# Optimization experiments

Hardware: AMD Instinct MI355X
Metric: run time of the kernel (lower is better)

The kernel has to match this reference:

```python
import jax, jax.numpy as jnp
import numpy as np

B, T, D, H = 16, 2048, 512, 512  # batch, seq_len, input_dim, hidden_dim


def setup_inputs() -> dict:
    key = jax.random.key(0)
    k1, k2, k3 = jax.random.split(key, 3)
    x = jax.random.normal(k1, (B, T, D), dtype=jnp.float32)
    # vanilla tanh RnnCell parameters
    W_xh = jax.random.normal(k2, (D, H), dtype=jnp.float32) / np.float32(np.sqrt(D))
    W_hh = jax.random.normal(k3, (H, H), dtype=jnp.float32) / np.float32(np.sqrt(H))
    b = jnp.zeros((H,), dtype=jnp.float32)
    # DFA feedback matrix, 'diagonal' init branch: diag(linspace(0,1,H))
    A = jnp.diag(jnp.linspace(0.0, 1.0, H).astype(jnp.float32))
    return {"x": x, "W_xh": W_xh, "W_hh": W_hh, "b": b, "A": A}


def reference(x, W_xh, W_hh, b, A):
    # Forward of DfaRnn: sequential RNN loop. detach() does not change forward
    # values, so this is a plain tanh RNN scan. A only affects the backward.
    Bb = x.shape[0]
    h0 = jnp.zeros((Bb, W_hh.shape[0]), dtype=x.dtype)

    def step(h, xt):
        h_new = jnp.tanh(xt @ W_xh + h @ W_hh + b)
        return h_new, h_new

    _, hs = jax.lax.scan(step, h0, jnp.swapaxes(x, 0, 1))  # [T,B,H]
    return jnp.swapaxes(hs, 0, 1)  # [B,T,H]
```

## Files before the change

### kernel.cpp

```cpp
#include <hip/hip_runtime.h>
#include <cmath>

#define B_ 16
#define T_ 2048
#define D_ 512
#define H_ 512

__global__ __launch_bounds__(256) void gemm_xw(
    const float* __restrict__ x,
    const float* __restrict__ Wxh,
    const float* __restrict__ bias,
    float* __restrict__ out)
{
    const int tid = threadIdx.x;
    const int n0 = blockIdx.x * 128;
    const int m0 = blockIdx.y * 128;

    __shared__ float As[8][132];
    __shared__ float Bs[8][132];

    const int tx = tid & 15, ty = tid >> 4;
    float acc[8][8] = {};

    const int arow = tid >> 1;
    const int akq  = (tid & 1) * 4;
    const int brow = tid >> 5;
    const int bcol = (tid & 31) * 4;

    for (int k0 = 0; k0 < D_; k0 += 8) {
        float4 a4 = *(const float4*)(x + (size_t)(m0 + arow) * D_ + k0 + akq);
        float4 b4 = *(const float4*)(Wxh + (size_t)(k0 + brow) * H_ + n0 + bcol);
        __syncthreads();
        As[akq + 0][arow] = a4.x;
        As[akq + 1][arow] = a4.y;
        As[akq + 2][arow] = a4.z;
        As[akq + 3][arow] = a4.w;
        *(float4*)(&Bs[brow][bcol]) = b4;
        __syncthreads();
#pragma unroll
        for (int kk = 0; kk < 8; ++kk) {
            float4 a0 = *(const float4*)(&As[kk][ty * 8]);
            float4 a1 = *(const float4*)(&As[kk][ty * 8 + 4]);
            float4 b0 = *(const float4*)(&Bs[kk][tx * 8]);
            float4 b1 = *(const float4*)(&Bs[kk][tx * 8 + 4]);
            float a_[8] = {a0.x, a0.y, a0.z, a0.w, a1.x, a1.y, a1.z, a1.w};
            float b_[8] = {b0.x, b0.y, b0.z, b0.w, b1.x, b1.y, b1.z, b1.w};
#pragma unroll
            for (int i = 0; i < 8; ++i)
#pragma unroll
                for (int j = 0; j < 8; ++j) acc[i][j] += a_[i] * b_[j];
        }
    }

    const float4 bv0 = *(const float4*)(bias + n0 + tx * 8);
    const float4 bv1 = *(const float4*)(bias + n0 + tx * 8 + 4);
    const float bb[8] = {bv0.x, bv0.y, bv0.z, bv0.w, bv1.x, bv1.y, bv1.z, bv1.w};
#pragma unroll
    for (int i = 0; i < 8; ++i) {
        const int m = m0 + ty * 8 + i;
        float4 o0, o1;
        o0.x = acc[i][0] + bb[0]; o0.y = acc[i][1] + bb[1];
        o0.z = acc[i][2] + bb[2]; o0.w = acc[i][3] + bb[3];
        o1.x = acc[i][4] + bb[4]; o1.y = acc[i][5] + bb[5];
        o1.z = acc[i][6] + bb[6]; o1.w = acc[i][7] + bb[7];
        *(float4*)(out + (size_t)m * H_ + n0 + tx * 8)     = o0;
        *(float4*)(out + (size_t)m * H_ + n0 + tx * 8 + 4) = o1;
    }
}

__device__ __forceinline__ void bar_lds() {
    asm volatile("s_waitcnt lgkmcnt(0)\n\ts_barrier" ::: "memory");
}

__global__ __launch_bounds__(512, 2) void rnn_rec(
    const float* __restrict__ Whh,
    float* __restrict__ out,
    unsigned long long* __restrict__ ws)
{
    const int tid = threadIdx.x;
    const int b = blockIdx.x & 15;
    const int s = blockIdx.x >> 4;
    const int j = tid & 63;
    const int p = tid >> 6;
    const int col = (s << 6) + j;

    __shared__ float h_lds[H_];
    __shared__ float part[8 * 64];

    float W_reg[64];
    {
        const float* wbase = Whh + (size_t)(p * 64) * H_ + col;
#pragma unroll
        for (int r = 0; r < 64; ++r) {
            const float* addr = wbase + (size_t)r * H_;
            asm volatile("global_load_dword %0, %1, off"
                         : "=v"(W_reg[r]) : "v"(addr));
        }
        asm volatile("s_waitcnt vmcnt(0)" ::: "memory");
    }

    h_lds[tid] = 0.0f;
    __syncthreads();

    float* outb = out + (size_t)b * T_ * H_;
    unsigned long long* wsb = ws + (size_t)b * 2 * H_;

    float xw0 = 0.0f, xw1 = 0.0f, xw2 = 0.0f;
    if (p == 0) {
        xw0 = outb[(size_t)0 * H_ + col];
        xw1 = outb[(size_t)1 * H_ + col];
        xw2 = outb[(size_t)2 * H_ + col];
    }

    for (int t = 0; t < T_; ++t) {
        float acc = 0.0f;
        const float4* hv = (const float4*)(h_lds + (p << 6));
#pragma unroll
        for (int i = 0; i < 16; ++i) {
            float4 h4 = hv[i];
            acc += h4.x * W_reg[4 * i + 0];
            acc += h4.y * W_reg[4 * i + 1];
            acc += h4.z * W_reg[4 * i + 2];
            acc += h4.w * W_reg[4 * i + 3];
        }
        part[tid] = acc;
        bar_lds();

        const unsigned int tag = (unsigned int)(t + 1);
        const int slot = (t + 1) & 1;
        unsigned long long* wslot = wsb + (size_t)slot * H_;

        if (p == 0) {
            asm volatile("s_waitcnt vmcnt(0)" ::: "memory");
            float ssum = xw0;
#pragma unroll
            for (int q = 0; q < 8; ++q) ssum += part[q * 64 + j];
            union { unsigned int u; float f; } cv;
            cv.f = tanhf(ssum);
            unsigned long long pv =
                ((unsigned long long)tag << 32) | (unsigned long long)cv.u;
            __hip_atomic_store(wslot + col, pv, __ATOMIC_RELAXED,
                               __HIP_MEMORY_SCOPE_AGENT);
            outb[(size_t)t * H_ + col] = cv.f;
            h_lds[col] = cv.f;
            xw0 = xw1;
            xw1 = xw2;
            xw2 = (t + 3 < T_) ? outb[(size_t)(t + 3) * H_ + col] : 0.0f;
        } else {
            const int q = (p == s) ? 0 : p;
            unsigned long long* src = wslot + (q << 6) + j;
            unsigned long long v;
            do {
                v = __hip_atomic_load(src, __ATOMIC_RELAXED,
                                      __HIP_MEMORY_SCOPE_AGENT);
            } while ((unsigned int)(v >> 32) < tag);
            union { unsigned int u; float f; } cv;
            cv.u = (unsigned int)v;
            h_lds[(q << 6) + j] = cv.f;
        }
        bar_lds();
    }
}

extern "C" void kernel_launch(void* const* d_in, const int* in_sizes, int n_in,
                              void* d_out, int out_size, void* d_ws,
                              size_t ws_size, hipStream_t stream) {
    const float* x    = (const float*)d_in[0];
    const float* Wxh  = (const float*)d_in[1];
    const float* Whh  = (const float*)d_in[2];
    const float* bias = (const float*)d_in[3];
    float* out = (float*)d_out;

    hipMemsetAsync(d_ws, 0, (size_t)B_ * 2 * H_ * sizeof(unsigned long long),
                   stream);

    dim3 ggrid(H_ / 128, (B_ * T_) / 128, 1);
    gemm_xw<<<ggrid, 256, 0, stream>>>(x, Wxh, bias, out);

    rnn_rec<<<128, 512, 0, stream>>>(Whh, out, (unsigned long long*)d_ws);
}
```

Baseline: 2.966 ms.

## Restructure RNN step to one barrier with a distributed shuffle reduction

The per-step recurrence is reorganised. Every wave now polls the global exchange buffer for its own 64-element slice of h at the start of the step, so each wave only reads h values it wrote itself and the second block barrier goes away. The cross-wave partial-sum reduction is spread over all waves using a transposed LDS read plus xor shuffles, rather than being done serially by wave 0. The partial buffer and the xw prefetch are double-buffered in LDS to stay safe with a single barrier. In exchange, every wave now polls global memory, and correctness depends on subtle LDS ordering across steps.

```diff
diff --git a/kernel.cpp b/kernel.cpp
--- a/kernel.cpp
+++ b/kernel.cpp
@@ -75,21 +75,21 @@
 __global__ __launch_bounds__(512, 2) void rnn_rec(
     const float* __restrict__ Whh,
     float* __restrict__ out,
-    unsigned long long* __restrict__ ws)
+    unsigned long long* __restrict__ ex)
 {
     const int tid = threadIdx.x;
     const int b = blockIdx.x & 15;
     const int s = blockIdx.x >> 4;
-    const int j = tid & 63;
+    const int l = tid & 63;
     const int p = tid >> 6;
-    const int col = (s << 6) + j;
 
     __shared__ float h_lds[H_];
-    __shared__ float part[8 * 64];
+    __shared__ float part[2][8 * 68];
+    __shared__ float xw_lds[2][64];
 
     float W_reg[64];
     {
-        const float* wbase = Whh + (size_t)(p * 64) * H_ + col;
+        const float* wbase = Whh + (size_t)(p * 64) * H_ + (s * 64 + l);
 #pragma unroll
         for (int r = 0; r < 64; ++r) {
             const float* addr = wbase + (size_t)r * H_;
@@ -99,20 +99,36 @@
         asm volatile("s_waitcnt vmcnt(0)" ::: "memory");
     }
 
+    float* outb = out + (size_t)b * T_ * H_;
+    unsigned long long* exb = ex + (size_t)b * 2 * H_;
+
     h_lds[tid] = 0.0f;
+    if (tid < 128) {
+        const int tt = tid >> 6;
+        const int c  = tid & 63;
+        xw_lds[tt][c] = outb[(size_t)tt * H_ + s * 64 + c];
+    }
     __syncthreads();
 
-    float* outb = out + (size_t)b * T_ * H_;
-    unsigned long long* wsb = ws + (size_t)b * 2 * H_;
-
-    float xw0 = 0.0f, xw1 = 0.0f, xw2 = 0.0f;
-    if (p == 0) {
-        xw0 = outb[(size_t)0 * H_ + col];
-        xw1 = outb[(size_t)1 * H_ + col];
-        xw2 = outb[(size_t)2 * H_ + col];
-    }
+    const int g    = l & 7;
+    const int cl   = p * 8 + (l >> 3);
+    const int gcol = s * 64 + cl;
 
     for (int t = 0; t < T_; ++t) {
+        if (t > 0) {
+            unsigned long long* src =
+                exb + (size_t)(t & 1) * H_ + (p << 6) + l;
+            unsigned long long v;
+            do {
+                v = __hip_atomic_load(src, __ATOMIC_RELAXED,
+                                      __HIP_MEMORY_SCOPE_AGENT);
+            } while ((unsigned int)(v >> 32) < (unsigned int)t);
+            union { unsigned int u; float f; } cv;
+            cv.u = (unsigned int)v;
+            h_lds[(p << 6) + l] = cv.f;
+            asm volatile("s_waitcnt lgkmcnt(0)" ::: "memory");
+        }
+
         float acc = 0.0f;
         const float4* hv = (const float4*)(h_lds + (p << 6));
 #pragma unroll
@@ -123,42 +139,29 @@
             acc += h4.z * W_reg[4 * i + 2];
             acc += h4.w * W_reg[4 * i + 3];
         }
-        part[tid] = acc;
+        part[t & 1][p * 68 + l] = acc;
         bar_lds();
 
+        float v = part[t & 1][g * 68 + cl];
+        v += __shfl_xor(v, 1);
+        v += __shfl_xor(v, 2);
+        v += __shfl_xor(v, 4);
+        v += xw_lds[t & 1][cl];
+        const float h = tanhf(v);
+
         const unsigned int tag = (unsigned int)(t + 1);
-        const int slot = (t + 1) & 1;
-        unsigned long long* wslot = wsb + (size_t)slot * H_;
-
-        if (p == 0) {
-            asm volatile("s_waitcnt vmcnt(0)" ::: "memory");
-            float ssum = xw0;
-#pragma unroll
-            for (int q = 0; q < 8; ++q) ssum += part[q * 64 + j];
+        if (g == 0) {
             union { unsigned int u; float f; } cv;
-            cv.f = tanhf(ssum);
+            cv.f = h;
             unsigned long long pv =
                 ((unsigned long long)tag << 32) | (unsigned long long)cv.u;
-            __hip_atomic_store(wslot + col, pv, __ATOMIC_RELAXED,
-                               __HIP_MEMORY_SCOPE_AGENT);
-            outb[(size_t)t * H_ + col] = cv.f;
-            h_lds[col] = cv.f;
-            xw0 = xw1;
-            xw1 = xw2;
-            xw2 = (t + 3 < T_) ? outb[(size_t)(t + 3) * H_ + col] : 0.0f;
-        } else {
-            const int q = (p == s) ? 0 : p;
-            unsigned long long* src = wslot + (q << 6) + j;
-            unsigned long long v;
-            do {
-                v = __hip_atomic_load(src, __ATOMIC_RELAXED,
-                                      __HIP_MEMORY_SCOPE_AGENT);
-            } while ((unsigned int)(v >> 32) < tag);
-            union { unsigned int u; float f; } cv;
-            cv.u = (unsigned int)v;
-            h_lds[(q << 6) + j] = cv.f;
+            __hip_atomic_store(exb + (size_t)(tag & 1) * H_ + gcol, pv,
+                               __ATOMIC_RELAXED, __HIP_MEMORY_SCOPE_AGENT);
+        } else if (g == 1) {
+            outb[(size_t)t * H_ + gcol] = h;
+        } else if (g == 2 && t + 2 < T_) {
+            xw_lds[t & 1][cl] = outb[(size_t)(t + 2) * H_ + gcol];
         }
-        bar_lds();
     }
 }
 
```

New measurement: 4.835 ms. 63.0% more time.
